# Kernel tuning notes

Measured on AMD Instinct MI355X. Metric: run time of the kernel, lower is better.

## Reference

```python
import jax, jax.numpy as jnp
import numpy as np

EPS = 1e-8  # torch cosine_similarity norm clamp

def _cos(a, b, axis=-1):
    na = jnp.maximum(jnp.linalg.norm(a, axis=axis), EPS)
    nb = jnp.maximum(jnp.linalg.norm(b, axis=axis), EPS)
    return jnp.sum(a * b, axis=axis) / (na * nb)

def setup_inputs() -> dict:
    key = jax.random.key(0)
    ks = jax.random.split(key, 9)
    B, L, D, S = 8, 8192, 512, 131072
    scale = 0.02
    x = jax.random.normal(ks[0], (B, L, D), jnp.float32)
    context_W = jax.random.normal(ks[1], (D, D), jnp.float32) * scale
    context_b = jnp.zeros((D,), jnp.float32)
    pred_W1 = jax.random.normal(ks[2], (D, D), jnp.float32) * scale
    pred_b1 = jnp.zeros((D,), jnp.float32)
    pred_W2 = jax.random.normal(ks[3], (D, D), jnp.float32) * scale
    pred_b2 = jnp.zeros((D,), jnp.float32)
    raw_embeddings = jax.random.normal(ks[4], (S, D), jnp.float32)
    u = jax.random.uniform(ks[5], (S,), jnp.float32)
    surprise_level = jnp.where(u > 0.5, u, 0.0)  # ~half the slots active
    return {"x": x, "context_W": context_W, "context_b": context_b,
            "pred_W1": pred_W1, "pred_b1": pred_b1,
            "pred_W2": pred_W2, "pred_b2": pred_b2,
            "raw_embeddings": raw_embeddings, "surprise_level": surprise_level}

def reference(x, context_W, context_b, pred_W1, pred_b1, pred_W2, pred_b2,
              raw_embeddings, surprise_level):
    # context = pad(x[:, :-1], left-shift by one along seq), i.e. causal previous token
    context = jnp.pad(x[:, :-1, :], ((0, 0), (1, 0), (0, 0)))
    # predictor MLP on projected context (torch Linear: y = x @ W.T + b)
    ctx = context @ context_W.T + context_b
    h = jax.nn.gelu(ctx @ pred_W1.T + pred_b1, approximate=False)
    prediction = h @ pred_W2.T + pred_b2  # [B, L, D]
    mse = jnp.mean((x - prediction) ** 2, axis=-1)
    prediction_surprise = jnp.sqrt(mse)  # [B, L]

    # memory-contrastive surprise: cosine sim of pooled x vs active stored embeddings
    active = surprise_level > 0  # [S]
    x_pooled = jnp.mean(x, axis=1)  # [B, D]
    sim = _cos(x_pooled[:, None, :], raw_embeddings[None, :, :])  # [B, S]
    sim = jnp.where(active[None, :], sim, -jnp.inf)
    max_sim = jnp.max(sim, axis=-1)           # [B]
    best_idx = jnp.argmax(sim, axis=-1)       # [B]
    best_stored = raw_embeddings[best_idx]    # [B, D] argmax-based gather
    divergence = 1.0 - _cos(x, best_stored[:, None, :])  # [B, L]
    pattern_match = (max_sim[:, None] > 0.3).astype(x.dtype)
    contrastive = pattern_match * divergence

    surprise = jnp.maximum(prediction_surprise, contrastive * 2.0)  # [B, L]
    return surprise
```

## Files before the change

kernel.cpp:

```cpp
#include <hip/hip_runtime.h>
#include <math.h>

#define OFF_SIMKEY   0
#define OFF_POOLED   1024
#define ZEROED_BYTES 17408
#define OFF_MAXSIM   17408
#define OFF_NORME    17664
#define OFF_EBEST    17920
#define OFF_BPRIME   34304
#define OFF_WP       36864
#define OFF_W2B      561152

typedef __attribute__((ext_vector_type(8))) short bf16x8;
typedef __attribute__((ext_vector_type(4))) float f32x4;

__device__ inline unsigned short f2bf(float f) {
    unsigned int u = __float_as_uint(f);
    unsigned int r = (u + 0x7FFFu + ((u >> 16) & 1u)) >> 16;
    return (unsigned short)r;
}

__device__ inline void load_lds_16(const void* g, void* l) {
    __builtin_amdgcn_global_load_lds((const __attribute__((address_space(1))) void*)g,
                                     (__attribute__((address_space(3))) void*)l, 16, 0, 0);
}

__global__ void __launch_bounds__(256) k_pre(const float* __restrict__ W1, const float* __restrict__ Wc,
                      const float* __restrict__ b1, const float* __restrict__ bc,
                      unsigned short* __restrict__ Wp, float* __restrict__ bprime) {
    __shared__ float w1row[512];
    __shared__ float wsum[4];
    int t = threadIdx.x;
    int n = blockIdx.x >> 1, half = blockIdx.x & 1;
    if (t < 128) ((float4*)w1row)[t] = ((const float4*)(W1 + (size_t)n * 512))[t];
    __syncthreads();
    int k = half * 256 + t;
    float acc = 0.f;
#pragma unroll 8
    for (int j = 0; j < 512; ++j) acc += w1row[j] * Wc[(size_t)j * 512 + k];
    Wp[(size_t)n * 512 + k] = f2bf(acc);
    if (half == 0) {
        float p = w1row[t] * bc[t] + w1row[t + 256] * bc[t + 256];
#pragma unroll
        for (int m = 32; m >= 1; m >>= 1) p += __shfl_xor(p, m);
        if ((t & 63) == 0) wsum[t >> 6] = p;
        __syncthreads();
        if (t == 0) bprime[n] = b1[n] + wsum[0] + wsum[1] + wsum[2] + wsum[3];
    }
}

__global__ void __launch_bounds__(256) k_cast(const float* __restrict__ W2, unsigned short* __restrict__ W2b) {
    int i = blockIdx.x * 1024 + threadIdx.x * 4;
    float4 v = *(const float4*)(W2 + i);
    ushort4 o;
    o.x = f2bf(v.x); o.y = f2bf(v.y); o.z = f2bf(v.z); o.w = f2bf(v.w);
    *(ushort4*)(W2b + i) = o;
}

__global__ void __launch_bounds__(512) k_pool(const float* __restrict__ x, float* __restrict__ pooled) {
    __shared__ float4 pb[4][128];
    int t = threadIdx.x;
    int q = t & 127;
    int rg = t >> 7;
    int b = blockIdx.y;
    int l0 = blockIdx.x * 128;
    const float4* p = (const float4*)(x + ((size_t)b * 8192 + l0 + rg) * 512) + q;
    float4 s = make_float4(0.f, 0.f, 0.f, 0.f);
#pragma unroll 8
    for (int i = 0; i < 32; ++i) {
        float4 v = p[(size_t)i * 512];
        s.x += v.x; s.y += v.y; s.z += v.z; s.w += v.w;
    }
    pb[rg][q] = s;
    __syncthreads();
    if (rg == 0) {
        float4 a = pb[0][q], b1_ = pb[1][q], c = pb[2][q], d = pb[3][q];
        atomicAdd(&pooled[b * 512 + q * 4 + 0], a.x + b1_.x + c.x + d.x);
        atomicAdd(&pooled[b * 512 + q * 4 + 1], a.y + b1_.y + c.y + d.y);
        atomicAdd(&pooled[b * 512 + q * 4 + 2], a.z + b1_.z + c.z + d.z);
        atomicAdd(&pooled[b * 512 + q * 4 + 3], a.w + b1_.w + c.w + d.w);
    }
}

__global__ void __launch_bounds__(256) k_sim(const float* __restrict__ E, const float* __restrict__ sl,
                     const float* __restrict__ pooledws, unsigned long long* __restrict__ simkey) {
    __shared__ float ps[4096];
    __shared__ unsigned long long wkey[4][8];
    int t = threadIdx.x, lane = t & 63, w = t >> 6;
#pragma unroll
    for (int c = 0; c < 16; ++c) ps[t + c * 256] = pooledws[t + c * 256] * (1.0f / 8192.0f);
    __syncthreads();
    float pr[8][8];
#pragma unroll
    for (int b = 0; b < 8; ++b) {
        float4 v0 = *(const float4*)&ps[b * 512 + lane * 8];
        float4 v1 = *(const float4*)&ps[b * 512 + lane * 8 + 4];
        pr[b][0] = v0.x; pr[b][1] = v0.y; pr[b][2] = v0.z; pr[b][3] = v0.w;
        pr[b][4] = v1.x; pr[b][5] = v1.y; pr[b][6] = v1.z; pr[b][7] = v1.w;
    }
    float npinv[8];
#pragma unroll
    for (int b = 0; b < 8; ++b) {
        float s = 0.f;
#pragma unroll
        for (int j = 0; j < 8; ++j) s += pr[b][j] * pr[b][j];
#pragma unroll
        for (int m = 32; m >= 1; m >>= 1) s += __shfl_xor(s, m);
        npinv[b] = 1.0f / fmaxf(sqrtf(s), 1e-8f);
    }
    unsigned long long best[8];
#pragma unroll
    for (int b = 0; b < 8; ++b) best[b] = 0ull;
    int sbase = blockIdx.x * 64 + w * 16;
    float mysl = (lane < 16) ? sl[sbase + lane] : 0.f;
    unsigned long long mask = __ballot(mysl > 0.0f);
    for (int it = 0; it < 16; ++it) {
        if (!((mask >> it) & 1ull)) continue;
        int s = sbase + it;
        const float4* ep = (const float4*)(E + (size_t)s * 512);
        float4 e0 = ep[lane * 2], e1 = ep[lane * 2 + 1];
        float nrm = e0.x * e0.x + e0.y * e0.y + e0.z * e0.z + e0.w * e0.w
                  + e1.x * e1.x + e1.y * e1.y + e1.z * e1.z + e1.w * e1.w;
        float dt[8];
#pragma unroll
        for (int b = 0; b < 8; ++b)
            dt[b] = e0.x * pr[b][0] + e0.y * pr[b][1] + e0.z * pr[b][2] + e0.w * pr[b][3]
                  + e1.x * pr[b][4] + e1.y * pr[b][5] + e1.z * pr[b][6] + e1.w * pr[b][7];
#pragma unroll
        for (int m = 32; m >= 1; m >>= 1) {
            nrm += __shfl_xor(nrm, m);
#pragma unroll
            for (int b = 0; b < 8; ++b) dt[b] += __shfl_xor(dt[b], m);
        }
        float neinv = 1.0f / fmaxf(sqrtf(nrm), 1e-8f);
#pragma unroll
        for (int b = 0; b < 8; ++b) {
            float sim = dt[b] * npinv[b] * neinv;
            unsigned int u = __float_as_uint(sim);
            unsigned int k32 = (u & 0x80000000u) ? ~u : (u | 0x80000000u);
            unsigned long long key = ((unsigned long long)k32 << 32) | (unsigned int)(~(unsigned int)s);
            if (key > best[b]) best[b] = key;
        }
    }
    if (lane == 0) {
#pragma unroll
        for (int b = 0; b < 8; ++b) wkey[w][b] = best[b];
    }
    __syncthreads();
    if (t < 8) {
        unsigned long long k = wkey[0][t];
#pragma unroll
        for (int w2 = 1; w2 < 4; ++w2) if (wkey[w2][t] > k) k = wkey[w2][t];
        if (k) atomicMax(&simkey[t], k);
    }
}

__global__ void __launch_bounds__(64) k_b2(const float* __restrict__ E, const unsigned long long* __restrict__ simkey,
                    float* __restrict__ max_sim, float* __restrict__ norm_e, float* __restrict__ ebest) {
    int b = blockIdx.x, lane = threadIdx.x;
    unsigned long long key = simkey[b];
    float ms; unsigned int idx;
    if (key == 0ull) { ms = -1e30f; idx = 0u; }
    else {
        unsigned int k32 = (unsigned int)(key >> 32);
        unsigned int u = (k32 & 0x80000000u) ? (k32 & 0x7FFFFFFFu) : ~k32;
        ms = __uint_as_float(u);
        idx = ~(unsigned int)(key & 0xFFFFFFFFull);
    }
    const float4* ep = (const float4*)(E + (size_t)idx * 512);
    float4 e0 = ep[lane * 2], e1 = ep[lane * 2 + 1];
    *(float4*)&ebest[b * 512 + lane * 8] = e0;
    *(float4*)&ebest[b * 512 + lane * 8 + 4] = e1;
    float s = e0.x * e0.x + e0.y * e0.y + e0.z * e0.z + e0.w * e0.w
            + e1.x * e1.x + e1.y * e1.y + e1.z * e1.z + e1.w * e1.w;
#pragma unroll
    for (int m = 32; m >= 1; m >>= 1) s += __shfl_xor(s, m);
    if (lane == 0) { max_sim[b] = ms; norm_e[b] = fmaxf(sqrtf(s), 1e-8f); }
}

__global__ void __launch_bounds__(512, 2) k_mega(
        const float* __restrict__ x, const unsigned short* __restrict__ Wp,
        const float* __restrict__ bprime, const unsigned short* __restrict__ W2b,
        const float* __restrict__ b2, const float* __restrict__ ebest,
        const float* __restrict__ max_sim, const float* __restrict__ norm_e,
        float* __restrict__ out) {
    __shared__ char smem[145408];
    unsigned short* Hs = (unsigned short*)(smem);
    unsigned short* Bs = (unsigned short*)(smem + 65536);
    unsigned int*  Ts32 = (unsigned int*)(smem + 131072);
    unsigned short* Ts = (unsigned short*)(smem + 131072);
    float* red = (float*)(smem + 139264);

    const int t = threadIdx.x;
    const int lane = t & 63, w = t >> 6;
    const int l15 = lane & 15, quad = lane >> 4;
    const int gr0 = blockIdx.x * 64;
    const int b = gr0 >> 13;

    int srcB[4];
#pragma unroll
    for (int c = 0; c < 4; ++c) {
        int off16 = c * 512 + t;
        int row = off16 >> 2, slot = off16 & 3;
        int g = slot ^ ((row >> 1) & 3);
        srcB[c] = row * 512 + g * 8;
    }
    const int r = t >> 3, cc = t & 7;
    const int sR = (r >> 1) & 3;
    const int d0 = (((cc >> 2) ^ sR) << 2) | (cc & 3);
    const int d1 = ((((cc >> 2) + 2) ^ sR) << 2) | (cc & 3);
    int tsoff[4], bsoff[4], hoff[4];
#pragma unroll
    for (int i = 0; i < 4; ++i) {
        int rowA = i * 16 + l15;
        tsoff[i] = rowA * 32 + ((quad ^ ((rowA >> 1) & 3)) << 3);
        hoff[i]  = rowA * 32 + ((quad ^ ((rowA >> 2) & 3)) << 3);
        int rowB = w * 64 + i * 16 + l15;
        bsoff[i] = rowB * 32 + ((quad ^ ((rowB >> 1) & 3)) << 3);
    }

    unsigned int alo[16], ahi[16];
    {
        int gr = gr0 + r;
        bool z = ((gr & 8191) == 0);
        const float* src = x + ((size_t)gr - 1) * 512 + cc * 2;
#pragma unroll
        for (int kt = 0; kt < 16; ++kt) {
            float2 v0 = make_float2(0.f, 0.f), v1 = make_float2(0.f, 0.f);
            if (!z) { v0 = *(const float2*)(src + kt * 32); v1 = *(const float2*)(src + kt * 32 + 16); }
            alo[kt] = (unsigned int)f2bf(v0.x) | ((unsigned int)f2bf(v0.y) << 16);
            ahi[kt] = (unsigned int)f2bf(v1.x) | ((unsigned int)f2bf(v1.y) << 16);
        }
    }

    Ts32[r * 16 + d0] = alo[0];
    Ts32[r * 16 + d1] = ahi[0];
#pragma unroll
    for (int c = 0; c < 4; ++c)
        load_lds_16(Wp + srcB[c], Bs + c * 4096 + w * 512);
    __syncthreads();

    f32x4 acc[4][4];
#pragma unroll
    for (int i = 0; i < 4; ++i)
#pragma unroll
        for (int j = 0; j < 4; ++j) acc[i][j] = (f32x4){0.f, 0.f, 0.f, 0.f};
#pragma unroll
    for (int kt = 0; kt < 16; ++kt) {
        const int cur = kt & 1, nxt = cur ^ 1;
        if (kt < 15) {
            Ts32[nxt * 1024 + r * 16 + d0] = alo[kt + 1];
            Ts32[nxt * 1024 + r * 16 + d1] = ahi[kt + 1];
#pragma unroll
            for (int c = 0; c < 4; ++c)
                load_lds_16(Wp + srcB[c] + (kt + 1) * 32, Bs + nxt * 16384 + c * 4096 + w * 512);
        } else {
#pragma unroll
            for (int c = 0; c < 4; ++c)
                load_lds_16(W2b + srcB[c], Bs + c * 4096 + w * 512);
        }
        bf16x8 af[4], bfr[4];
#pragma unroll
        for (int i = 0; i < 4; ++i) af[i] = *(const bf16x8*)&Ts[cur * 2048 + tsoff[i]];
#pragma unroll
        for (int j = 0; j < 4; ++j) bfr[j] = *(const bf16x8*)&Bs[cur * 16384 + bsoff[j]];
#pragma unroll
        for (int i = 0; i < 4; ++i)
#pragma unroll
            for (int j = 0; j < 4; ++j)
                acc[i][j] = __builtin_amdgcn_mfma_f32_16x16x32_bf16(af[i], bfr[j], acc[i][j], 0, 0, 0);
        __syncthreads();
    }

    {
        float bpj[4];
#pragma unroll
        for (int j = 0; j < 4; ++j) bpj[j] = bprime[w * 64 + j * 16 + l15];
#pragma unroll
        for (int i = 0; i < 4; ++i)
#pragma unroll
            for (int j = 0; j < 4; ++j)
#pragma unroll
                for (int rg = 0; rg < 4; ++rg) {
                    int m = i * 16 + quad * 4 + rg;
                    int ktc = w * 2 + (j >> 1);
                    int grp = ((j & 1) * 2 + (l15 >> 3)) ^ ((m >> 2) & 3);
                    float v = acc[i][j][rg] + bpj[j];
                    v = 0.5f * v * (1.0f + erff(v * 0.70710678118f));
                    Hs[ktc * 2048 + m * 32 + grp * 8 + (l15 & 7)] = f2bf(v);
                }
    }
    __syncthreads();

    f32x4 acc2[4][4];
#pragma unroll
    for (int i = 0; i < 4; ++i)
#pragma unroll
        for (int j = 0; j < 4; ++j) acc2[i][j] = (f32x4){0.f, 0.f, 0.f, 0.f};
#pragma unroll
    for (int kt = 0; kt < 16; ++kt) {
        const int cur = kt & 1, nxt = cur ^ 1;
        if (kt < 15) {
#pragma unroll
            for (int c = 0; c < 4; ++c)
                load_lds_16(W2b + srcB[c] + (kt + 1) * 32, Bs + nxt * 16384 + c * 4096 + w * 512);
        }
        bf16x8 af[4], bfr[4];
#pragma unroll
        for (int i = 0; i < 4; ++i) af[i] = *(const bf16x8*)&Hs[kt * 2048 + hoff[i]];
#pragma unroll
        for (int j = 0; j < 4; ++j) bfr[j] = *(const bf16x8*)&Bs[cur * 16384 + bsoff[j]];
#pragma unroll
        for (int i = 0; i < 4; ++i)
#pragma unroll
            for (int j = 0; j < 4; ++j)
                acc2[i][j] = __builtin_amdgcn_mfma_f32_16x16x32_bf16(af[i], bfr[j], acc2[i][j], 0, 0, 0);
        if (kt < 15) __syncthreads();
    }

    {
        float b2j[4], ej[4];
#pragma unroll
        for (int j = 0; j < 4; ++j) {
            int n = w * 64 + j * 16 + l15;
            b2j[j] = b2[n];
            ej[j] = ebest[b * 512 + n];
        }
#pragma unroll
        for (int i = 0; i < 4; ++i)
#pragma unroll
            for (int rg = 0; rg < 4; ++rg) {
                int m = i * 16 + quad * 4 + rg;
                int gr = gr0 + m;
                float sd = 0.f, sx = 0.f, sdt = 0.f;
#pragma unroll
                for (int j = 0; j < 4; ++j) {
                    int n = w * 64 + j * 16 + l15;
                    float p = acc2[i][j][rg] + b2j[j];
                    float xv = x[(size_t)gr * 512 + n];
                    float d = xv - p;
                    sd += d * d; sx += xv * xv; sdt += xv * ej[j];
                }
#pragma unroll
                for (int mm = 8; mm >= 1; mm >>= 1) {
                    sd += __shfl_xor(sd, mm);
                    sx += __shfl_xor(sx, mm);
                    sdt += __shfl_xor(sdt, mm);
                }
                if (l15 == 0) {
                    red[(m * 8 + w) * 3 + 0] = sd;
                    red[(m * 8 + w) * 3 + 1] = sx;
                    red[(m * 8 + w) * 3 + 2] = sdt;
                }
            }
    }
    __syncthreads();
    if (t < 64) {
        float sd = 0.f, sx = 0.f, sdt = 0.f;
#pragma unroll
        for (int w2 = 0; w2 < 8; ++w2) {
            sd  += red[(t * 8 + w2) * 3 + 0];
            sx  += red[(t * 8 + w2) * 3 + 1];
            sdt += red[(t * 8 + w2) * 3 + 2];
        }
        float ps = sqrtf(sd * (1.0f / 512.0f));
        float ms = max_sim[b];
        float c = 0.f;
        if (ms > 0.3f) {
            float nx = fmaxf(sqrtf(sx), 1e-8f);
            c = 2.0f * (1.0f - sdt / (nx * norm_e[b]));
        }
        out[gr0 + t] = fmaxf(ps, c);
    }
}

extern "C" void kernel_launch(void* const* d_in, const int* in_sizes, int n_in,
                              void* d_out, int out_size, void* d_ws, size_t ws_size,
                              hipStream_t stream) {
    const float* x  = (const float*)d_in[0];
    const float* Wc = (const float*)d_in[1];
    const float* bc = (const float*)d_in[2];
    const float* W1 = (const float*)d_in[3];
    const float* b1 = (const float*)d_in[4];
    const float* W2 = (const float*)d_in[5];
    const float* b2 = (const float*)d_in[6];
    const float* E  = (const float*)d_in[7];
    const float* sl = (const float*)d_in[8];

    char* ws = (char*)d_ws;
    unsigned long long* simkey = (unsigned long long*)(ws + OFF_SIMKEY);
    float* pooled  = (float*)(ws + OFF_POOLED);
    float* max_sim = (float*)(ws + OFF_MAXSIM);
    float* norm_e  = (float*)(ws + OFF_NORME);
    float* ebest   = (float*)(ws + OFF_EBEST);
    float* bprime  = (float*)(ws + OFF_BPRIME);
    unsigned short* Wp  = (unsigned short*)(ws + OFF_WP);
    unsigned short* W2b = (unsigned short*)(ws + OFF_W2B);
    float* out = (float*)d_out;

    hipMemsetAsync(ws, 0, ZEROED_BYTES, stream);
    k_pre<<<1024, 256, 0, stream>>>(W1, Wc, b1, bc, Wp, bprime);
    k_cast<<<256, 256, 0, stream>>>(W2, W2b);
    k_pool<<<dim3(64, 8), 512, 0, stream>>>(x, pooled);
    k_sim<<<2048, 256, 0, stream>>>(E, sl, pooled, simkey);
    k_b2<<<8, 64, 0, stream>>>(E, simkey, max_sim, norm_e, ebest);
    k_mega<<<1024, 512, 0, stream>>>(x, Wp, bprime, W2b, b2, ebest, max_sim, norm_e, out);
}
```

Baseline: 658.9 us.

## Load GEMM weight fragments directly from global instead of staging through LDS

Weight (B) fragments for both MLP GEMMs are now read straight from global memory (L2-cached) per wave, and the LDS double-buffer with global_load_lds and per-k-step barriers is removed. The whole bf16 context tile is written to LDS up front. The aim is to drop the per-iteration __syncthreads and free LDS. The cost is that each wave now does global-latency loads inside the MFMA loop with no explicit prefetch, and weight traffic to L2 goes up.

After: 695.8 us. 1.06x slower.

```diff
diff --git a/kernel.cpp b/kernel.cpp
--- a/kernel.cpp
+++ b/kernel.cpp
@@ -18,11 +18,6 @@
     unsigned int u = __float_as_uint(f);
     unsigned int r = (u + 0x7FFFu + ((u >> 16) & 1u)) >> 16;
     return (unsigned short)r;
-}
-
-__device__ inline void load_lds_16(const void* g, void* l) {
-    __builtin_amdgcn_global_load_lds((const __attribute__((address_space(1))) void*)g,
-                                     (__attribute__((address_space(3))) void*)l, 16, 0, 0);
 }
 
 __global__ void __launch_bounds__(256) k_pre(const float* __restrict__ W1, const float* __restrict__ Wc,
@@ -184,12 +179,11 @@
         const float* __restrict__ b2, const float* __restrict__ ebest,
         const float* __restrict__ max_sim, const float* __restrict__ norm_e,
         float* __restrict__ out) {
-    __shared__ char smem[145408];
-    unsigned short* Hs = (unsigned short*)(smem);
-    unsigned short* Bs = (unsigned short*)(smem + 65536);
-    unsigned int*  Ts32 = (unsigned int*)(smem + 131072);
-    unsigned short* Ts = (unsigned short*)(smem + 131072);
-    float* red = (float*)(smem + 139264);
+    __shared__ char smem[137216];
+    unsigned int*   Ts32 = (unsigned int*)(smem);
+    unsigned short* Ts   = (unsigned short*)(smem);
+    unsigned short* Hs   = (unsigned short*)(smem + 65536);
+    float*          red  = (float*)(smem + 131072);
 
     const int t = threadIdx.x;
     const int lane = t & 63, w = t >> 6;
@@ -197,29 +191,28 @@
     const int gr0 = blockIdx.x * 64;
     const int b = gr0 >> 13;
 
-    int srcB[4];
-#pragma unroll
-    for (int c = 0; c < 4; ++c) {
-        int off16 = c * 512 + t;
-        int row = off16 >> 2, slot = off16 & 3;
-        int g = slot ^ ((row >> 1) & 3);
-        srcB[c] = row * 512 + g * 8;
-    }
     const int r = t >> 3, cc = t & 7;
     const int sR = (r >> 1) & 3;
     const int d0 = (((cc >> 2) ^ sR) << 2) | (cc & 3);
     const int d1 = ((((cc >> 2) + 2) ^ sR) << 2) | (cc & 3);
-    int tsoff[4], bsoff[4], hoff[4];
+
+    int tsoff[4], hoff[4];
 #pragma unroll
     for (int i = 0; i < 4; ++i) {
         int rowA = i * 16 + l15;
         tsoff[i] = rowA * 32 + ((quad ^ ((rowA >> 1) & 3)) << 3);
         hoff[i]  = rowA * 32 + ((quad ^ ((rowA >> 2) & 3)) << 3);
-        int rowB = w * 64 + i * 16 + l15;
-        bsoff[i] = rowB * 32 + ((quad ^ ((rowB >> 1) & 3)) << 3);
-    }
-
-    unsigned int alo[16], ahi[16];
+    }
+
+    const unsigned short* bp1[4];
+    const unsigned short* bp2[4];
+#pragma unroll
+    for (int j = 0; j < 4; ++j) {
+        int n = w * 64 + j * 16 + l15;
+        bp1[j] = Wp  + n * 512 + quad * 8;
+        bp2[j] = W2b + n * 512 + quad * 8;
+    }
+
     {
         int gr = gr0 + r;
         bool z = ((gr & 8191) == 0);
@@ -228,16 +221,10 @@
         for (int kt = 0; kt < 16; ++kt) {
             float2 v0 = make_float2(0.f, 0.f), v1 = make_float2(0.f, 0.f);
             if (!z) { v0 = *(const float2*)(src + kt * 32); v1 = *(const float2*)(src + kt * 32 + 16); }
-            alo[kt] = (unsigned int)f2bf(v0.x) | ((unsigned int)f2bf(v0.y) << 16);
-            ahi[kt] = (unsigned int)f2bf(v1.x) | ((unsigned int)f2bf(v1.y) << 16);
-        }
-    }
-
-    Ts32[r * 16 + d0] = alo[0];
-    Ts32[r * 16 + d1] = ahi[0];
-#pragma unroll
-    for (int c = 0; c < 4; ++c)
-        load_lds_16(Wp + srcB[c], Bs + c * 4096 + w * 512);
+            Ts32[kt * 1024 + r * 16 + d0] = (unsigned int)f2bf(v0.x) | ((unsigned int)f2bf(v0.y) << 16);
+            Ts32[kt * 1024 + r * 16 + d1] = (unsigned int)f2bf(v1.x) | ((unsigned int)f2bf(v1.y) << 16);
+        }
+    }
     __syncthreads();
 
     f32x4 acc[4][4];
@@ -247,29 +234,16 @@
         for (int j = 0; j < 4; ++j) acc[i][j] = (f32x4){0.f, 0.f, 0.f, 0.f};
 #pragma unroll
     for (int kt = 0; kt < 16; ++kt) {
-        const int cur = kt & 1, nxt = cur ^ 1;
-        if (kt < 15) {
-            Ts32[nxt * 1024 + r * 16 + d0] = alo[kt + 1];
-            Ts32[nxt * 1024 + r * 16 + d1] = ahi[kt + 1];
-#pragma unroll
-            for (int c = 0; c < 4; ++c)
-                load_lds_16(Wp + srcB[c] + (kt + 1) * 32, Bs + nxt * 16384 + c * 4096 + w * 512);
-        } else {
-#pragma unroll
-            for (int c = 0; c < 4; ++c)
-                load_lds_16(W2b + srcB[c], Bs + c * 4096 + w * 512);
-        }
         bf16x8 af[4], bfr[4];
 #pragma unroll
-        for (int i = 0; i < 4; ++i) af[i] = *(const bf16x8*)&Ts[cur * 2048 + tsoff[i]];
-#pragma unroll
-        for (int j = 0; j < 4; ++j) bfr[j] = *(const bf16x8*)&Bs[cur * 16384 + bsoff[j]];
+        for (int i = 0; i < 4; ++i) af[i] = *(const bf16x8*)&Ts[kt * 2048 + tsoff[i]];
+#pragma unroll
+        for (int j = 0; j < 4; ++j) bfr[j] = *(const bf16x8*)(bp1[j] + kt * 32);
 #pragma unroll
         for (int i = 0; i < 4; ++i)
 #pragma unroll
             for (int j = 0; j < 4; ++j)
                 acc[i][j] = __builtin_amdgcn_mfma_f32_16x16x32_bf16(af[i], bfr[j], acc[i][j], 0, 0, 0);
-        __syncthreads();
     }
 
     {
@@ -299,23 +273,16 @@
         for (int j = 0; j < 4; ++j) acc2[i][j] = (f32x4){0.f, 0.f, 0.f, 0.f};
 #pragma unroll
     for (int kt = 0; kt < 16; ++kt) {
-        const int cur = kt & 1, nxt = cur ^ 1;
-        if (kt < 15) {
-#pragma unroll
-            for (int c = 0; c < 4; ++c)
-                load_lds_16(W2b + srcB[c] + (kt + 1) * 32, Bs + nxt * 16384 + c * 4096 + w * 512);
-        }
         bf16x8 af[4], bfr[4];
 #pragma unroll
         for (int i = 0; i < 4; ++i) af[i] = *(const bf16x8*)&Hs[kt * 2048 + hoff[i]];
 #pragma unroll
-        for (int j = 0; j < 4; ++j) bfr[j] = *(const bf16x8*)&Bs[cur * 16384 + bsoff[j]];
+        for (int j = 0; j < 4; ++j) bfr[j] = *(const bf16x8*)(bp2[j] + kt * 32);
 #pragma unroll
         for (int i = 0; i < 4; ++i)
 #pragma unroll
             for (int j = 0; j < 4; ++j)
                 acc2[i][j] = __builtin_amdgcn_mfma_f32_16x16x32_bf16(af[i], bfr[j], acc2[i][j], 0, 0, 0);
-        if (kt < 15) __syncthreads();
     }
 
     {
```
